# Optimization experiments

Hardware: AMD Instinct MI355X
Metric: run time of the kernel (lower is better)

## Reference

```python
import jax, jax.numpy as jnp
import numpy as np

B, T, D, H = 128, 1024, 128, 512

def setup_inputs() -> dict:
    key = jax.random.key(0)
    ks = jax.random.split(key, 7)
    s = 1.0 / np.sqrt(H)
    return {
        "x":    jax.random.normal(ks[0], (B, T, D), dtype=jnp.float32),
        "W_ih": jax.random.uniform(ks[1], (4 * H, D), jnp.float32, -s, s),
        "W_hh": jax.random.uniform(ks[2], (4 * H, H), jnp.float32, -s, s),
        "b_ih": jax.random.uniform(ks[3], (4 * H,), jnp.float32, -s, s),
        "b_hh": jax.random.uniform(ks[4], (4 * H,), jnp.float32, -s, s),
        "W_fc": jax.random.uniform(ks[5], (1, H), jnp.float32, -s, s),
        "b_fc": jax.random.uniform(ks[6], (1,), jnp.float32, -s, s),
    }

def _lstm_last_hidden(x, W_ih, W_hh, b_ih, b_hh):
    # Precompute input-side gate projections for all timesteps: [T, B, 4H]
    xg = jnp.einsum('btd,gd->tbg', x, W_ih) + (b_ih + b_hh)
    Bq = x.shape[0]
    Hq = W_hh.shape[1]
    h0 = jnp.zeros((Bq, Hq), x.dtype)
    c0 = jnp.zeros((Bq, Hq), x.dtype)

    def step(carry, g_in):
        h, c = carry
        g = g_in + h @ W_hh.T                      # [B, 4H]
        i, f, gc, o = jnp.split(g, 4, axis=-1)     # PyTorch gate order i,f,g,o
        i = jax.nn.sigmoid(i)
        f = jax.nn.sigmoid(f)
        gc = jnp.tanh(gc)
        o = jax.nn.sigmoid(o)
        c = f * c + i * gc
        h = o * jnp.tanh(c)
        return (h, c), None

    (h_last, _), _ = jax.lax.scan(step, (h0, c0), xg)
    return h_last

def reference(x, W_ih, W_hh, b_ih, b_hh, W_fc, b_fc):
    h = _lstm_last_hidden(x, W_ih, W_hh, b_ih, b_hh)   # out[:, -1, :]
    return jax.nn.sigmoid(h @ W_fc.T + b_fc)           # [B, 1]
```

## Files before the change

### kernel.cpp

```cpp
#include <hip/hip_runtime.h>
#include <hip/hip_bf16.h>

#define Bsz 128
#define Tsz 1024
#define Dsz 128
#define Hsz 512
#define NBLK 256
#define NKC 20

typedef __attribute__((ext_vector_type(8))) short short8;
typedef __attribute__((ext_vector_type(4))) float f4;
typedef unsigned long long u64;

__device__ __forceinline__ short bf16_rne(float f) {
  unsigned u = __builtin_bit_cast(unsigned, f);
  u += 0x7fffu + ((u >> 16) & 1u);
  return (short)(u >> 16);
}
__device__ __forceinline__ float sigmoid_(float v) { return 1.f / (1.f + __expf(-v)); }
__device__ __forceinline__ float tanh_fast(float v) {
  return 1.f - 2.f / (1.f + __expf(2.f * v));
}

__global__ __launch_bounds__(256, 1) void lstm_persist(
    const float* __restrict__ x, const float* __restrict__ W_ih,
    const float* __restrict__ W_hh, const float* __restrict__ b_ih,
    const float* __restrict__ b_hh, const float* __restrict__ W_fc,
    const float* __restrict__ b_fc, float* __restrict__ out,
    int* flags, unsigned short* hb0, unsigned short* hb1)
{
  const int bx = blockIdx.x;
  const int bt = bx & 7, ks = bx >> 3;
  const int b0 = bt << 4, k0 = ks << 4;
  const int tx = threadIdx.x;
  const int wave = tx >> 6, lane = tx & 63;
  const int m = lane & 15, quad = lane >> 4;
  const int k_l = tx & 15, b_l = tx >> 4;

  __shared__ short8 A_lds[NKC][64];
  __shared__ f4 gates_lds[4][64];
  __shared__ float fc_red[16][16];

  int* gflags = flags + bt * 32;

  short8 wfrag[NKC];
  {
    const int j = wave * Hsz + k0 + m;
    #pragma unroll
    for (int kc = 0; kc < NKC; ++kc) {
      const int kk = kc * 32 + quad * 8;
      const float* src = (kk < Dsz) ? (W_ih + (size_t)j * Dsz + kk)
                                    : (W_hh + (size_t)j * Hsz + (kk - Dsz));
      const f4* sv = (const f4*)src;
      f4 v0 = sv[0], v1 = sv[1];
      short8 w;
      w[0] = bf16_rne(v0[0]); w[1] = bf16_rne(v0[1]);
      w[2] = bf16_rne(v0[2]); w[3] = bf16_rne(v0[3]);
      w[4] = bf16_rne(v1[0]); w[5] = bf16_rne(v1[1]);
      w[6] = bf16_rne(v1[2]); w[7] = bf16_rne(v1[3]);
      wfrag[kc] = w;
    }
  }
  float bias[4];
  #pragma unroll
  for (int g = 0; g < 4; ++g)
    bias[g] = b_ih[g * Hsz + k0 + k_l] + b_hh[g * Hsz + k0 + k_l];
  float c_reg = 0.f;

  for (int t = 0; t < Tsz; ++t) {
    unsigned short* hnext = (t & 1) ? hb1 : hb0;
    const unsigned short* hprev = (t & 1) ? hb0 : hb1;

    const f4* xv = (const f4*)(x + (size_t)(b0 + m) * (Tsz * Dsz)
                               + (size_t)t * Dsz + wave * 32 + quad * 8);
    f4 v0 = xv[0], v1 = xv[1];

    if (t > 0) {
      for (;;) {
        int f = __hip_atomic_load(gflags + (lane & 31),
                                  __ATOMIC_RELAXED, __HIP_MEMORY_SCOPE_AGENT);
        if (__all(f >= t)) break;
        __builtin_amdgcn_s_sleep(1);
      }
      #pragma unroll
      for (int q = 0; q < 4; ++q) {
        const int kc = 4 + wave * 4 + q;
        const int kh = (kc - 4) * 32 + quad * 8;
        const u64* p = (const u64*)(hprev + (size_t)(b0 + m) * Hsz + kh);
        u64 lo = __hip_atomic_load(p,     __ATOMIC_RELAXED, __HIP_MEMORY_SCOPE_AGENT);
        u64 hi = __hip_atomic_load(p + 1, __ATOMIC_RELAXED, __HIP_MEMORY_SCOPE_AGENT);
        u64* dst = (u64*)&A_lds[kc][lane];
        dst[0] = lo; dst[1] = hi;
      }
    } else {
      short8 z = {0, 0, 0, 0, 0, 0, 0, 0};
      #pragma unroll
      for (int q = 0; q < 4; ++q) A_lds[4 + wave * 4 + q][lane] = z;
    }

    {
      short8 a;
      a[0] = bf16_rne(v0[0]); a[1] = bf16_rne(v0[1]);
      a[2] = bf16_rne(v0[2]); a[3] = bf16_rne(v0[3]);
      a[4] = bf16_rne(v1[0]); a[5] = bf16_rne(v1[1]);
      a[6] = bf16_rne(v1[2]); a[7] = bf16_rne(v1[3]);
      A_lds[wave][lane] = a;
    }
    __syncthreads();

    f4 a0 = {0.f, 0.f, 0.f, 0.f}, a1 = {0.f, 0.f, 0.f, 0.f};
    f4 a2 = {0.f, 0.f, 0.f, 0.f}, a3 = {0.f, 0.f, 0.f, 0.f};
    #pragma unroll
    for (int kc = 0; kc < NKC; kc += 4) {
      a0 = __builtin_amdgcn_mfma_f32_16x16x32_bf16(A_lds[kc][lane],     wfrag[kc],     a0, 0, 0, 0);
      a1 = __builtin_amdgcn_mfma_f32_16x16x32_bf16(A_lds[kc + 1][lane], wfrag[kc + 1], a1, 0, 0, 0);
      a2 = __builtin_amdgcn_mfma_f32_16x16x32_bf16(A_lds[kc + 2][lane], wfrag[kc + 2], a2, 0, 0, 0);
      a3 = __builtin_amdgcn_mfma_f32_16x16x32_bf16(A_lds[kc + 3][lane], wfrag[kc + 3], a3, 0, 0, 0);
    }
    gates_lds[wave][lane] = (a0 + a1) + (a2 + a3);
    __syncthreads();

    {
      const int lp = ((b_l >> 2) << 4) + k_l;
      const int r = b_l & 3;
      float pi = gates_lds[0][lp][r] + bias[0];
      float pf = gates_lds[1][lp][r] + bias[1];
      float pg = gates_lds[2][lp][r] + bias[2];
      float po = gates_lds[3][lp][r] + bias[3];
      float iv = sigmoid_(pi), fv = sigmoid_(pf), ov = sigmoid_(po);
      float gv = tanh_fast(pg);
      c_reg = fv * c_reg + iv * gv;
      float hv = ov * tanh_fast(c_reg);
      unsigned hbits = (unsigned)(unsigned short)bf16_rne(hv);
      unsigned obits = __shfl_xor(hbits, 1);
      if ((k_l & 1) == 0) {
        unsigned packed = hbits | (obits << 16);
        unsigned* p = (unsigned*)(hnext + (size_t)(b0 + b_l) * Hsz + k0 + k_l);
        __hip_atomic_store(p, packed, __ATOMIC_RELAXED, __HIP_MEMORY_SCOPE_AGENT);
      }
    }
    __syncthreads();
    if (tx == 0)
      __hip_atomic_store(gflags + ks, t + 1, __ATOMIC_RELAXED, __HIP_MEMORY_SCOPE_AGENT);
  }

  if (ks == 0) {
    for (;;) {
      int f = __hip_atomic_load(gflags + (lane & 31),
                                __ATOMIC_RELAXED, __HIP_MEMORY_SCOPE_AGENT);
      if (__all(f >= Tsz)) break;
      __builtin_amdgcn_s_sleep(1);
    }
    const unsigned short* hl = hb1;
    const u64* p = (const u64*)(hl + (size_t)(b0 + b_l) * Hsz + k_l * 32);
    float partial = 0.f;
    #pragma unroll
    for (int q = 0; q < 8; ++q) {
      u64 v = __hip_atomic_load(p + q, __ATOMIC_RELAXED, __HIP_MEMORY_SCOPE_AGENT);
      #pragma unroll
      for (int e = 0; e < 4; ++e) {
        unsigned hv16 = (unsigned)((v >> (16 * e)) & 0xffffu);
        partial += __builtin_bit_cast(float, hv16 << 16) * W_fc[k_l * 32 + q * 4 + e];
      }
    }
    fc_red[b_l][k_l] = partial;
    __syncthreads();
    if (k_l == 0) {
      float s = b_fc[0];
      #pragma unroll
      for (int e = 0; e < 16; ++e) s += fc_red[b_l][e];
      out[b0 + b_l] = sigmoid_(s);
    }
  }
}

extern "C" void kernel_launch(void* const* d_in, const int* in_sizes, int n_in,
                              void* d_out, int out_size, void* d_ws, size_t ws_size,
                              hipStream_t stream) {
  const float* x    = (const float*)d_in[0];
  const float* W_ih = (const float*)d_in[1];
  const float* W_hh = (const float*)d_in[2];
  const float* b_ih = (const float*)d_in[3];
  const float* b_hh = (const float*)d_in[4];
  const float* W_fc = (const float*)d_in[5];
  const float* b_fc = (const float*)d_in[6];
  float* out = (float*)d_out;
  char* ws = (char*)d_ws;
  int* flags = (int*)ws;
  unsigned short* hb0 = (unsigned short*)(ws + 4096);
  unsigned short* hb1 = (unsigned short*)(ws + 4096 + (size_t)Bsz * Hsz * 2);
  hipMemsetAsync(ws, 0, 4096, stream);
  lstm_persist<<<NBLK, 256, 0, stream>>>(x, W_ih, W_hh, b_ih, b_hh, W_fc, b_fc,
                                         out, flags, hb0, hb1);
}
```

Before: 3.142 ms.

## Permute weight columns so gate nonlinearity runs from MFMA registers via shuffles

Rearranges the W fragment rows so each wave's 16 output columns hold all four gates for four hidden units. The gate values are then gathered across lanes with two xor-shuffle stages instead of a round trip through LDS. This removes one __syncthreads and the LDS gate buffer from the per-timestep critical path. h is now written as 64-bit packed stores from a quarter of the lanes instead of 32-bit stores.

```diff
diff --git a/kernel.cpp b/kernel.cpp
--- a/kernel.cpp
+++ b/kernel.cpp
@@ -38,14 +38,14 @@
   const int k_l = tx & 15, b_l = tx >> 4;
 
   __shared__ short8 A_lds[NKC][64];
-  __shared__ f4 gates_lds[4][64];
   __shared__ float fc_red[16][16];
 
   int* gflags = flags + bt * 32;
 
+  const int mycol = k0 + wave * 4 + (m & 3);
   short8 wfrag[NKC];
   {
-    const int j = wave * Hsz + k0 + m;
+    const int j = (m >> 2) * Hsz + mycol;
     #pragma unroll
     for (int kc = 0; kc < NKC; ++kc) {
       const int kk = kc * 32 + quad * 8;
@@ -64,7 +64,7 @@
   float bias[4];
   #pragma unroll
   for (int g = 0; g < 4; ++g)
-    bias[g] = b_ih[g * Hsz + k0 + k_l] + b_hh[g * Hsz + k0 + k_l];
+    bias[g] = b_ih[g * Hsz + mycol] + b_hh[g * Hsz + mycol];
   float c_reg = 0.f;
 
   for (int t = 0; t < Tsz; ++t) {
@@ -117,26 +117,35 @@
       a2 = __builtin_amdgcn_mfma_f32_16x16x32_bf16(A_lds[kc + 2][lane], wfrag[kc + 2], a2, 0, 0, 0);
       a3 = __builtin_amdgcn_mfma_f32_16x16x32_bf16(A_lds[kc + 3][lane], wfrag[kc + 3], a3, 0, 0, 0);
     }
-    gates_lds[wave][lane] = (a0 + a1) + (a2 + a3);
-    __syncthreads();
+    f4 acc = (a0 + a1) + (a2 + a3);
 
     {
-      const int lp = ((b_l >> 2) << 4) + k_l;
-      const int r = b_l & 3;
-      float pi = gates_lds[0][lp][r] + bias[0];
-      float pf = gates_lds[1][lp][r] + bias[1];
-      float pg = gates_lds[2][lp][r] + bias[2];
-      float po = gates_lds[3][lp][r] + bias[3];
+      const int g0b = (m >> 2) & 1, g1b = (m >> 3) & 1;
+      float s1[4], v1[4];
+      #pragma unroll
+      for (int r = 0; r < 4; ++r) s1[r] = __shfl_xor(acc[r ^ 1], 4);
+      #pragma unroll
+      for (int r = 0; r < 4; ++r) v1[r] = ((r & 1) == g0b) ? acc[r] : s1[r];
+      float s2[4], v2[4];
+      #pragma unroll
+      for (int r = 0; r < 4; ++r) s2[r] = __shfl_xor(v1[r ^ 2], 8);
+      #pragma unroll
+      for (int r = 0; r < 4; ++r) v2[r] = (((r >> 1) & 1) == g1b) ? v1[r] : s2[r];
+      float pi = v2[0] + bias[0];
+      float pf = v2[1] + bias[1];
+      float pg = v2[2] + bias[2];
+      float po = v2[3] + bias[3];
       float iv = sigmoid_(pi), fv = sigmoid_(pf), ov = sigmoid_(po);
       float gv = tanh_fast(pg);
       c_reg = fv * c_reg + iv * gv;
       float hv = ov * tanh_fast(c_reg);
       unsigned hbits = (unsigned)(unsigned short)bf16_rne(hv);
-      unsigned obits = __shfl_xor(hbits, 1);
-      if ((k_l & 1) == 0) {
-        unsigned packed = hbits | (obits << 16);
-        unsigned* p = (unsigned*)(hnext + (size_t)(b0 + b_l) * Hsz + k0 + k_l);
-        __hip_atomic_store(p, packed, __ATOMIC_RELAXED, __HIP_MEMORY_SCOPE_AGENT);
+      unsigned lo = hbits | (__shfl_xor(hbits, 1) << 16);
+      u64 both = ((u64)__shfl_xor(lo, 2) << 32) | (u64)lo;
+      if ((m & 3) == 0) {
+        const int brow = b0 + quad * 4 + (m >> 2);
+        u64* p = (u64*)(hnext + (size_t)brow * Hsz + k0 + wave * 4);
+        __hip_atomic_store(p, both, __ATOMIC_RELAXED, __HIP_MEMORY_SCOPE_AGENT);
       }
     }
     __syncthreads();
```

Result: no change. 3.167 ms (+0.8%).
